# Optimization experiments

Hardware: AMD Instinct MI355X
Metric: run time of the kernel (lower is better)

The kernel has to match this reference:

```python
import jax, jax.numpy as jnp
import numpy as np

NUM_HEADS = 8


def setup_inputs() -> dict:
    key = jax.random.key(0)
    ks = jax.random.split(key, 8)
    B, S, D = 2, 4096, 512
    # Linear weights init uniform(-0.1, 0.1), no bias; stored as [in, out]
    u = lambda k, shp: jax.random.uniform(k, shp, jnp.float32, -0.1, 0.1)
    return {
        "query_antecedent": jax.random.normal(ks[0], (B, S, D), jnp.float32),
        "memory_antecedent": jax.random.normal(ks[1], (B, S, D), jnp.float32),
        "bias": jax.random.normal(ks[2], (1, S, S), jnp.float32),
        "Wq": u(ks[3], (D, D)),
        "Wk": u(ks[4], (D, D)),
        "Wv": u(ks[5], (D, D)),
        "Wo": u(ks[6], (D, D)),
    }


def reference(query_antecedent, memory_antecedent, bias, Wq, Wk, Wv, Wo):
    B, S, D = query_antecedent.shape
    H = NUM_HEADS
    hd = D // H
    scale = hd ** (-0.5)
    q = (query_antecedent @ Wq) * scale              # [B,S,D]
    k = memory_antecedent @ Wk                       # [B,S,D]
    v = memory_antecedent @ Wv                       # [B,S,D]
    q = q.reshape(B, S, H, hd)
    k = k.reshape(B, S, H, hd)
    v = v.reshape(B, S, H, hd)
    # per-head logits with shared bias (broadcast over batch and heads)
    logits = jnp.einsum("bqhd,bkhd->bhqk", q, k) + bias[:, None, :, :]
    weights = jax.nn.softmax(logits, axis=-1)        # [B,H,S,S]
    out = jnp.einsum("bhqk,bkhd->bqhd", weights, v).reshape(B, S, D)
    return out @ Wo
```

## Files before the change

### kernel.cpp

```cpp
#include <hip/hip_runtime.h>
#include <hip/hip_bf16.h>

typedef __attribute__((ext_vector_type(8))) __bf16 bf16x8;
typedef __attribute__((ext_vector_type(4))) __bf16 bf16x4;
typedef __attribute__((ext_vector_type(4))) float f32x4;

#define LOG2E 1.4426950408889634f
#define FIXED_M 16.0f

static __device__ __forceinline__ f32x4 mfma16(bf16x8 a, bf16x8 b, f32x4 c) {
  return __builtin_amdgcn_mfma_f32_16x16x32_bf16(a, b, c, 0, 0, 0);
}

static __device__ __forceinline__ void gload_lds16(const void* g, void* l) {
  __builtin_amdgcn_global_load_lds(
      (const __attribute__((address_space(1))) unsigned int*)g,
      (__attribute__((address_space(3))) unsigned int*)l, 16, 0, 0);
}

__global__ __launch_bounds__(256) void k_cvt(const float* __restrict__ in,
                                             __bf16* __restrict__ out, int n4) {
  for (int i = blockIdx.x * blockDim.x + threadIdx.x; i < n4;
       i += gridDim.x * blockDim.x) {
    float4 v = reinterpret_cast<const float4*>(in)[i];
    bf16x4 o = {(__bf16)v.x, (__bf16)v.y, (__bf16)v.z, (__bf16)v.w};
    reinterpret_cast<bf16x4*>(out)[i] = o;
  }
}

__global__ __launch_bounds__(256) void k_wt(const float* __restrict__ W,
                                            __bf16* __restrict__ Wt) {
  __shared__ float tile[64][65];
  int bx = blockIdx.x;
  int by = blockIdx.y;
  int tid = threadIdx.x;
#pragma unroll
  for (int p = 0; p < 16; p++) {
    int idx = p * 256 + tid;
    int r = idx >> 6, c = idx & 63;
    tile[r][c] = W[(size_t)(by * 64 + r) * 512 + bx * 64 + c];
  }
  __syncthreads();
#pragma unroll
  for (int p = 0; p < 16; p++) {
    int idx = p * 256 + tid;
    int rn = idx >> 6, ck = idx & 63;
    Wt[(size_t)(bx * 64 + rn) * 512 + by * 64 + ck] = (__bf16)tile[ck][rn];
  }
}

template <int OUT_MODE>
__global__ __launch_bounds__(256) void k_gemm(const __bf16* __restrict__ A,
                                              const __bf16* __restrict__ Bt,
                                              void* __restrict__ Cout,
                                              float scale) {
  constexpr bool SWAP = (OUT_MODE != 2);
  __shared__ __bf16 As[128][72];
  __shared__ __bf16 Bs[64][72];
  const int tid = threadIdx.x;
  const int wid = tid >> 6, lane = tid & 63;
  const int g = lane >> 4, c = lane & 15;
  const int m0 = blockIdx.x * 128, n0 = blockIdx.y * 64;
  const int wr = wid >> 1, wc = wid & 1;

  f32x4 acc[4][2];
#pragma unroll
  for (int i = 0; i < 4; i++)
#pragma unroll
    for (int j = 0; j < 2; j++) acc[i][j] = (f32x4){0.f, 0.f, 0.f, 0.f};

  for (int k0 = 0; k0 < 512; k0 += 64) {
#pragma unroll
    for (int q = 0; q < 4; q++) {
      int idx = (q * 256 + tid) * 8;
      int r = idx >> 6, cc = idx & 63;
      bf16x8 v = *reinterpret_cast<const bf16x8*>(A + (size_t)(m0 + r) * 512 + k0 + cc);
      *reinterpret_cast<bf16x8*>(&As[r][cc]) = v;
    }
#pragma unroll
    for (int q = 0; q < 2; q++) {
      int idx = (q * 256 + tid) * 8;
      int r = idx >> 6, cc = idx & 63;
      bf16x8 v = *reinterpret_cast<const bf16x8*>(Bt + (size_t)(n0 + r) * 512 + k0 + cc);
      *reinterpret_cast<bf16x8*>(&Bs[r][cc]) = v;
    }
    __syncthreads();
#pragma unroll
    for (int kk = 0; kk < 2; kk++) {
      bf16x8 bfrag[2];
#pragma unroll
      for (int nf = 0; nf < 2; nf++)
        bfrag[nf] = *reinterpret_cast<const bf16x8*>(&Bs[wc * 32 + nf * 16 + c][kk * 32 + g * 8]);
#pragma unroll
      for (int mf = 0; mf < 4; mf++) {
        bf16x8 afrag = *reinterpret_cast<const bf16x8*>(&As[wr * 64 + mf * 16 + c][kk * 32 + g * 8]);
#pragma unroll
        for (int nf = 0; nf < 2; nf++)
          acc[mf][nf] = SWAP ? mfma16(bfrag[nf], afrag, acc[mf][nf])
                             : mfma16(afrag, bfrag[nf], acc[mf][nf]);
      }
    }
    __syncthreads();
  }
#pragma unroll
  for (int mf = 0; mf < 4; mf++)
#pragma unroll
    for (int nf = 0; nf < 2; nf++) {
      if (OUT_MODE == 0) {
        int mm = m0 + wr * 64 + mf * 16 + c;
        int nnb = n0 + wc * 32 + nf * 16 + g * 4;
        int b = mm >> 12, s = mm & 4095, h = nnb >> 6, d = nnb & 63;
        bf16x4 ov = {(__bf16)(acc[mf][nf][0] * scale), (__bf16)(acc[mf][nf][1] * scale),
                     (__bf16)(acc[mf][nf][2] * scale), (__bf16)(acc[mf][nf][3] * scale)};
        *reinterpret_cast<bf16x4*>((__bf16*)Cout + ((((size_t)b * 8 + h) * 4096) + s) * 64 + d) = ov;
      } else if (OUT_MODE == 1) {
        int mm = m0 + wr * 64 + mf * 16 + c;
        int nnb = n0 + wc * 32 + nf * 16 + g * 4;
        f32x4 ov = acc[mf][nf] * scale;
        *reinterpret_cast<f32x4*>((float*)Cout + (size_t)mm * 512 + nnb) = ov;
      } else {
        int mmb = m0 + wr * 64 + mf * 16 + g * 4;
        int nn = n0 + wc * 32 + nf * 16 + c;
        int b = mmb >> 12, s = mmb & 4095, h = nn >> 6, d = nn & 63;
        bf16x4 ov = {(__bf16)(acc[mf][nf][0] * scale), (__bf16)(acc[mf][nf][1] * scale),
                     (__bf16)(acc[mf][nf][2] * scale), (__bf16)(acc[mf][nf][3] * scale)};
        *reinterpret_cast<bf16x4*>((__bf16*)Cout + (((size_t)b * 8 + h) * 64 + d) * 4096 + s) = ov;
      }
    }
}

__global__ __launch_bounds__(256, 2) void k_attn(const __bf16* __restrict__ Q,
                                                 const __bf16* __restrict__ K,
                                                 const __bf16* __restrict__ Vt,
                                                 const float* __restrict__ bias,
                                                 __bf16* __restrict__ Out) {
  __shared__ __bf16 KVs[2][2][64][64];
  __shared__ __bf16 Pl[4][2][16][64];

  const int qb = blockIdx.x, bh = blockIdx.y;
  const int b = bh >> 3, h = bh & 7;
  const int tid = threadIdx.x, wid = tid >> 6, lane = tid & 63;
  const int g = lane >> 4, c = lane & 15;
  const int swz = (c & 7) << 4;
  const char* Kb = (const char*)(K + (size_t)bh * 4096 * 64);
  const char* Vb = (const char*)(Vt + (size_t)bh * 64 * 4096);
  const __bf16* Qh = Q + (size_t)bh * 4096 * 64;
  const int q0 = qb * 128 + wid * 32;
  const int myq0 = q0 + c, myq1 = q0 + 16 + c;

  auto stage = [&](int db, int chunk) {
    const int reg = wid >> 1;
    char* dst0 = (char*)&KVs[db][reg][0][0] + (wid & 1) * 4096;
#pragma unroll
    for (int j = 0; j < 4; j++) {
      int Lp = (wid & 1) * 4096 + j * 1024 + lane * 16;
      int L = Lp ^ (((Lp >> 7) & 7) << 4);
      const char* src = (reg == 0)
          ? Kb + (size_t)chunk * 8192 + L
          : Vb + (size_t)(L >> 7) * 8192 + (size_t)chunk * 128 + (L & 127);
      gload_lds16(src, dst0 + j * 1024);
    }
  };

  const float* brow0 = bias + (size_t)myq0 * 4096;
  const float* brow1 = bias + (size_t)myq1 * 4096;

#define LOADB(dst, chunk)                                                      \
  {                                                                            \
    _Pragma("unroll") for (int f = 0; f < 4; f++) dst[0][f] =                  \
        *reinterpret_cast<const f32x4*>(brow0 + (chunk) * 64 + f * 16 + g * 4);\
    _Pragma("unroll") for (int f = 0; f < 4; f++) dst[1][f] =                  \
        *reinterpret_cast<const f32x4*>(brow1 + (chunk) * 64 + f * 16 + g * 4);\
  }

  bf16x8 qa[2][2];
  qa[0][0] = *reinterpret_cast<const bf16x8*>(Qh + (size_t)myq0 * 64 + g * 8);
  qa[0][1] = *reinterpret_cast<const bf16x8*>(Qh + (size_t)myq0 * 64 + 32 + g * 8);
  qa[1][0] = *reinterpret_cast<const bf16x8*>(Qh + (size_t)myq1 * 64 + g * 8);
  qa[1][1] = *reinterpret_cast<const bf16x8*>(Qh + (size_t)myq1 * 64 + 32 + g * 8);

  f32x4 lacc[2];
  lacc[0] = (f32x4){0.f, 0.f, 0.f, 0.f};
  lacc[1] = (f32x4){0.f, 0.f, 0.f, 0.f};
  f32x4 o[2][4];
#pragma unroll
  for (int qt = 0; qt < 2; qt++)
#pragma unroll
    for (int f = 0; f < 4; f++) o[qt][f] = (f32x4){0.f, 0.f, 0.f, 0.f};

  f32x4 bA[2][4], bB[2][4];
  const float NM = -FIXED_M * LOG2E;

  auto process = [&](int db, f32x4 (&bv)[2][4]) {
    asm volatile("s_waitcnt vmcnt(12)" ::: "memory");
    __builtin_amdgcn_s_barrier();
    const char* Kl = (const char*)&KVs[db][0][0][0];
    const char* Vl = (const char*)&KVs[db][1][0][0];
    f32x4 st[2][4];
    __builtin_amdgcn_s_setprio(1);
#pragma unroll
    for (int f = 0; f < 4; f++) {
      const char* rb = Kl + (f * 16 + c) * 128;
      bf16x8 k0 = *reinterpret_cast<const bf16x8*>(rb + ((g * 16) ^ swz));
      bf16x8 k1 = *reinterpret_cast<const bf16x8*>(rb + ((64 + g * 16) ^ swz));
      st[0][f] = mfma16(k1, qa[0][1], mfma16(k0, qa[0][0], bv[0][f]));
      st[1][f] = mfma16(k1, qa[1][1], mfma16(k0, qa[1][0], bv[1][f]));
    }
    __builtin_amdgcn_s_setprio(0);
#pragma unroll
    for (int qt = 0; qt < 2; qt++) {
      char* Pw = (char*)&Pl[wid][qt][0][0] + c * 128;
#pragma unroll
      for (int f = 0; f < 4; f++) {
#pragma unroll
        for (int r = 0; r < 4; r++)
          st[qt][f][r] = __builtin_exp2f(__builtin_fmaf(st[qt][f][r], LOG2E, NM));
        lacc[qt] += st[qt][f];
        bf16x4 pk = {(__bf16)st[qt][f][0], (__bf16)st[qt][f][1],
                     (__bf16)st[qt][f][2], (__bf16)st[qt][f][3]};
        *reinterpret_cast<bf16x4*>(Pw + ((f * 32 + g * 8) ^ swz)) = pk;
      }
    }
    __builtin_amdgcn_s_setprio(1);
#pragma unroll
    for (int kk = 0; kk < 2; kk++) {
      bf16x8 pb0 = *reinterpret_cast<const bf16x8*>(
          (char*)&Pl[wid][0][0][0] + c * 128 + ((kk * 64 + g * 16) ^ swz));
      bf16x8 pb1 = *reinterpret_cast<const bf16x8*>(
          (char*)&Pl[wid][1][0][0] + c * 128 + ((kk * 64 + g * 16) ^ swz));
#pragma unroll
      for (int fd = 0; fd < 4; fd++) {
        const char* rb = Vl + (fd * 16 + c) * 128;
        bf16x8 va = *reinterpret_cast<const bf16x8*>(rb + ((kk * 64 + g * 16) ^ swz));
        o[0][fd] = mfma16(va, pb0, o[0][fd]);
        o[1][fd] = mfma16(va, pb1, o[1][fd]);
      }
    }
    __builtin_amdgcn_s_setprio(0);
    __builtin_amdgcn_s_barrier();
  };

  stage(0, 0);
  asm volatile("" ::: "memory");
  stage(1, 1);
  asm volatile("" ::: "memory");
  LOADB(bA, 0);
  asm volatile("" ::: "memory");
  LOADB(bB, 1);
  asm volatile("" ::: "memory");

  for (int t = 0; t < 64; t += 2) {
    process(0, bA);
    stage(0, (t + 2) & 63);
    asm volatile("" ::: "memory");
    LOADB(bA, ((t + 2) & 63));
    asm volatile("" ::: "memory");
    process(1, bB);
    stage(1, (t + 3) & 63);
    asm volatile("" ::: "memory");
    LOADB(bB, ((t + 3) & 63));
    asm volatile("" ::: "memory");
  }

#pragma unroll
  for (int qt = 0; qt < 2; qt++) {
    float l = lacc[qt][0] + lacc[qt][1] + lacc[qt][2] + lacc[qt][3];
    l += __shfl_xor(l, 16);
    l += __shfl_xor(l, 32);
    float inv = 1.f / l;
    int myq = (qt == 0) ? myq0 : myq1;
    __bf16* Orow = Out + ((size_t)b * 4096 + myq) * 512 + h * 64;
#pragma unroll
    for (int fd = 0; fd < 4; fd++) {
      bf16x4 ov = {(__bf16)(o[qt][fd][0] * inv), (__bf16)(o[qt][fd][1] * inv),
                   (__bf16)(o[qt][fd][2] * inv), (__bf16)(o[qt][fd][3] * inv)};
      *reinterpret_cast<bf16x4*>(Orow + fd * 16 + g * 4) = ov;
    }
  }
#undef LOADB
}

extern "C" void kernel_launch(void* const* d_in, const int* in_sizes, int n_in,
                              void* d_out, int out_size, void* d_ws, size_t ws_size,
                              hipStream_t stream) {
  const float* xq = (const float*)d_in[0];
  const float* xm = (const float*)d_in[1];
  const float* bias = (const float*)d_in[2];
  const float* Wq = (const float*)d_in[3];
  const float* Wk = (const float*)d_in[4];
  const float* Wv = (const float*)d_in[5];
  const float* Wo = (const float*)d_in[6];

  const size_t MB = 1024 * 1024;
  char* ws = (char*)d_ws;
  __bf16* xq_b = (__bf16*)(ws + 0);
  __bf16* xm_b = (__bf16*)(ws + 8 * MB);
  __bf16* wqt = (__bf16*)(ws + 16 * MB);
  __bf16* wkt = (__bf16*)(ws + 16 * MB + 524288);
  __bf16* wvt = (__bf16*)(ws + 17 * MB);
  __bf16* wot = (__bf16*)(ws + 17 * MB + 524288);
  __bf16* Qb = (__bf16*)(ws + 18 * MB);
  __bf16* Kb = (__bf16*)(ws + 26 * MB);
  __bf16* Vtb = (__bf16*)(ws + 42 * MB);
  __bf16* AOb = (__bf16*)(ws + 50 * MB);
  if (ws_size < 58 * MB) return;

  const int n4 = 8192 * 512 / 4;
  k_cvt<<<2048, 256, 0, stream>>>(xq, xq_b, n4);
  k_cvt<<<2048, 256, 0, stream>>>(xm, xm_b, n4);
  k_wt<<<dim3(8, 8), 256, 0, stream>>>(Wq, wqt);
  k_wt<<<dim3(8, 8), 256, 0, stream>>>(Wk, wkt);
  k_wt<<<dim3(8, 8), 256, 0, stream>>>(Wv, wvt);
  k_wt<<<dim3(8, 8), 256, 0, stream>>>(Wo, wot);

  k_gemm<0><<<dim3(64, 8), 256, 0, stream>>>(xq_b, wqt, Qb, 0.125f);
  k_gemm<0><<<dim3(64, 8), 256, 0, stream>>>(xm_b, wkt, Kb, 1.0f);
  k_gemm<2><<<dim3(64, 8), 256, 0, stream>>>(xm_b, wvt, Vtb, 1.0f);

  k_attn<<<dim3(32, 16), 256, 0, stream>>>(Qb, Kb, Vtb, bias, AOb);

  k_gemm<1><<<dim3(64, 8), 256, 0, stream>>>(AOb, wot, d_out, 1.0f);
}
```

Before: 233.6 us.

## Split attention over key range into two halves with a reduction kernel

The attention grid gains a z dimension that splits the 4096 keys into two halves. Each block writes unnormalized bf16 partial outputs and row sums, and a new reduction kernel adds the halves and normalizes. The P tile in shared memory shrinks to one query tile per wave and launch bounds rise to 4 blocks per SM to raise occupancy. The workspace is reused to hold the partials. The cost is an extra launch, more global traffic for the partials, and bf16 rounding of the unnormalized partials.

```diff
diff --git a/kernel.cpp b/kernel.cpp
--- a/kernel.cpp
+++ b/kernel.cpp
@@ -129,16 +129,17 @@
     }
 }
 
-__global__ __launch_bounds__(256, 2) void k_attn(const __bf16* __restrict__ Q,
+__global__ __launch_bounds__(256, 4) void k_attn(const __bf16* __restrict__ Q,
                                                  const __bf16* __restrict__ K,
                                                  const __bf16* __restrict__ Vt,
                                                  const float* __restrict__ bias,
-                                                 __bf16* __restrict__ Out) {
+                                                 __bf16* __restrict__ Opart,
+                                                 float* __restrict__ lpart) {
   __shared__ __bf16 KVs[2][2][64][64];
-  __shared__ __bf16 Pl[4][2][16][64];
-
-  const int qb = blockIdx.x, bh = blockIdx.y;
-  const int b = bh >> 3, h = bh & 7;
+  __shared__ __bf16 Pl[4][16][64];
+
+  const int qb = blockIdx.x, bh = blockIdx.y, kh = blockIdx.z;
+  const int kb0 = kh * 32;
   const int tid = threadIdx.x, wid = tid >> 6, lane = tid & 63;
   const int g = lane >> 4, c = lane & 15;
   const int swz = (c & 7) << 4;
@@ -207,9 +208,9 @@
       st[1][f] = mfma16(k1, qa[1][1], mfma16(k0, qa[1][0], bv[1][f]));
     }
     __builtin_amdgcn_s_setprio(0);
+    char* Pw = (char*)&Pl[wid][0][0] + c * 128;
 #pragma unroll
     for (int qt = 0; qt < 2; qt++) {
-      char* Pw = (char*)&Pl[wid][qt][0][0] + c * 128;
 #pragma unroll
       for (int f = 0; f < 4; f++) {
 #pragma unroll
@@ -220,45 +221,41 @@
                      (__bf16)st[qt][f][2], (__bf16)st[qt][f][3]};
         *reinterpret_cast<bf16x4*>(Pw + ((f * 32 + g * 8) ^ swz)) = pk;
       }
-    }
-    __builtin_amdgcn_s_setprio(1);
-#pragma unroll
-    for (int kk = 0; kk < 2; kk++) {
-      bf16x8 pb0 = *reinterpret_cast<const bf16x8*>(
-          (char*)&Pl[wid][0][0][0] + c * 128 + ((kk * 64 + g * 16) ^ swz));
-      bf16x8 pb1 = *reinterpret_cast<const bf16x8*>(
-          (char*)&Pl[wid][1][0][0] + c * 128 + ((kk * 64 + g * 16) ^ swz));
-#pragma unroll
-      for (int fd = 0; fd < 4; fd++) {
-        const char* rb = Vl + (fd * 16 + c) * 128;
-        bf16x8 va = *reinterpret_cast<const bf16x8*>(rb + ((kk * 64 + g * 16) ^ swz));
-        o[0][fd] = mfma16(va, pb0, o[0][fd]);
-        o[1][fd] = mfma16(va, pb1, o[1][fd]);
+      __builtin_amdgcn_s_setprio(1);
+#pragma unroll
+      for (int kk = 0; kk < 2; kk++) {
+        bf16x8 pb = *reinterpret_cast<const bf16x8*>(Pw + ((kk * 64 + g * 16) ^ swz));
+#pragma unroll
+        for (int fd = 0; fd < 4; fd++) {
+          const char* rb = Vl + (fd * 16 + c) * 128;
+          bf16x8 va = *reinterpret_cast<const bf16x8*>(rb + ((kk * 64 + g * 16) ^ swz));
+          o[qt][fd] = mfma16(va, pb, o[qt][fd]);
+        }
       }
-    }
-    __builtin_amdgcn_s_setprio(0);
+      __builtin_amdgcn_s_setprio(0);
+    }
     __builtin_amdgcn_s_barrier();
   };
 
-  stage(0, 0);
+  stage(0, kb0 + 0);
   asm volatile("" ::: "memory");
-  stage(1, 1);
+  stage(1, kb0 + 1);
   asm volatile("" ::: "memory");
-  LOADB(bA, 0);
+  LOADB(bA, kb0 + 0);
   asm volatile("" ::: "memory");
-  LOADB(bB, 1);
+  LOADB(bB, kb0 + 1);
   asm volatile("" ::: "memory");
 
-  for (int t = 0; t < 64; t += 2) {
+  for (int t = 0; t < 32; t += 2) {
     process(0, bA);
-    stage(0, (t + 2) & 63);
+    stage(0, kb0 + ((t + 2) & 31));
     asm volatile("" ::: "memory");
-    LOADB(bA, ((t + 2) & 63));
+    LOADB(bA, kb0 + ((t + 2) & 31));
     asm volatile("" ::: "memory");
     process(1, bB);
-    stage(1, (t + 3) & 63);
+    stage(1, kb0 + ((t + 3) & 31));
     asm volatile("" ::: "memory");
-    LOADB(bB, ((t + 3) & 63));
+    LOADB(bB, kb0 + ((t + 3) & 31));
     asm volatile("" ::: "memory");
   }
 
@@ -267,17 +264,40 @@
     float l = lacc[qt][0] + lacc[qt][1] + lacc[qt][2] + lacc[qt][3];
     l += __shfl_xor(l, 16);
     l += __shfl_xor(l, 32);
-    float inv = 1.f / l;
     int myq = (qt == 0) ? myq0 : myq1;
-    __bf16* Orow = Out + ((size_t)b * 4096 + myq) * 512 + h * 64;
+    __bf16* Oprow = Opart + (((size_t)kh * 16 + bh) * 4096 + myq) * 64;
 #pragma unroll
     for (int fd = 0; fd < 4; fd++) {
-      bf16x4 ov = {(__bf16)(o[qt][fd][0] * inv), (__bf16)(o[qt][fd][1] * inv),
-                   (__bf16)(o[qt][fd][2] * inv), (__bf16)(o[qt][fd][3] * inv)};
-      *reinterpret_cast<bf16x4*>(Orow + fd * 16 + g * 4) = ov;
-    }
+      bf16x4 ov = {(__bf16)o[qt][fd][0], (__bf16)o[qt][fd][1],
+                   (__bf16)o[qt][fd][2], (__bf16)o[qt][fd][3]};
+      *reinterpret_cast<bf16x4*>(Oprow + fd * 16 + g * 4) = ov;
+    }
+    if (g == 0) lpart[((size_t)kh * 16 + bh) * 4096 + myq] = l;
   }
 #undef LOADB
+}
+
+__global__ __launch_bounds__(256) void k_red(const __bf16* __restrict__ Op,
+                                             const float* __restrict__ lp,
+                                             __bf16* __restrict__ AO) {
+  int i = blockIdx.x * 256 + threadIdx.x;
+  int bh = i >> 16;
+  int rem = i & 65535;
+  int s = rem >> 4;
+  int d4 = (rem & 15) << 2;
+  int b = bh >> 3, h = bh & 7;
+  size_t base0 = ((size_t)bh * 4096 + s) * 64 + d4;
+  size_t base1 = ((size_t)(16 + bh) * 4096 + s) * 64 + d4;
+  bf16x4 a = *reinterpret_cast<const bf16x4*>(Op + base0);
+  bf16x4 cc = *reinterpret_cast<const bf16x4*>(Op + base1);
+  float la = lp[(size_t)bh * 4096 + s];
+  float lb = lp[(size_t)(16 + bh) * 4096 + s];
+  float inv = 1.f / (la + lb);
+  bf16x4 ov = {(__bf16)(((float)a[0] + (float)cc[0]) * inv),
+               (__bf16)(((float)a[1] + (float)cc[1]) * inv),
+               (__bf16)(((float)a[2] + (float)cc[2]) * inv),
+               (__bf16)(((float)a[3] + (float)cc[3]) * inv)};
+  *reinterpret_cast<bf16x4*>(AO + ((size_t)b * 4096 + s) * 512 + h * 64 + d4) = ov;
 }
 
 extern "C" void kernel_launch(void* const* d_in, const int* in_sizes, int n_in,
@@ -295,15 +315,17 @@
   char* ws = (char*)d_ws;
   __bf16* xq_b = (__bf16*)(ws + 0);
   __bf16* xm_b = (__bf16*)(ws + 8 * MB);
+  __bf16* Opart = (__bf16*)(ws + 0);
   __bf16* wqt = (__bf16*)(ws + 16 * MB);
+  float* lpart = (float*)(ws + 16 * MB);
   __bf16* wkt = (__bf16*)(ws + 16 * MB + 524288);
   __bf16* wvt = (__bf16*)(ws + 17 * MB);
   __bf16* wot = (__bf16*)(ws + 17 * MB + 524288);
   __bf16* Qb = (__bf16*)(ws + 18 * MB);
   __bf16* Kb = (__bf16*)(ws + 26 * MB);
+  __bf16* AOb = (__bf16*)(ws + 34 * MB);
   __bf16* Vtb = (__bf16*)(ws + 42 * MB);
-  __bf16* AOb = (__bf16*)(ws + 50 * MB);
-  if (ws_size < 58 * MB) return;
+  if (ws_size < 50 * MB) return;
 
   const int n4 = 8192 * 512 / 4;
   k_cvt<<<2048, 256, 0, stream>>>(xq, xq_b, n4);
@@ -317,7 +339,8 @@
   k_gemm<0><<<dim3(64, 8), 256, 0, stream>>>(xm_b, wkt, Kb, 1.0f);
   k_gemm<2><<<dim3(64, 8), 256, 0, stream>>>(xm_b, wvt, Vtb, 1.0f);
 
-  k_attn<<<dim3(32, 16), 256, 0, stream>>>(Qb, Kb, Vtb, bias, AOb);
+  k_attn<<<dim3(32, 16, 2), 256, 0, stream>>>(Qb, Kb, Vtb, bias, Opart, lpart);
+  k_red<<<4096, 256, 0, stream>>>(Opart, lpart, AOb);
 
   k_gemm<1><<<dim3(64, 8), 256, 0, stream>>>(AOb, wot, d_out, 1.0f);
 }
```

New measurement: 537.0 us. +129.8%, slower.

## Replace LDS-staged attention with single-wave blocks loading K/V directly into registers

Applied to the files above, without the earlier changes.

Rewrites the attention kernel to use 64-thread blocks, each handling 32 queries. K, V and bias fragments now go straight from global memory into registers with double buffering, replacing the global-to-LDS staging, barriers and 64-key chunks with 32-key chunks. Block ids are remapped so neighbouring blocks cover different heads. This removes block-wide barriers and LDS traffic for K/V, but blocks no longer share K/V in LDS, so global and L2 load traffic rises. Workspace layout is also shrunk.

```diff
diff --git a/kernel.cpp b/kernel.cpp
--- a/kernel.cpp
+++ b/kernel.cpp
@@ -10,12 +10,6 @@
 
 static __device__ __forceinline__ f32x4 mfma16(bf16x8 a, bf16x8 b, f32x4 c) {
   return __builtin_amdgcn_mfma_f32_16x16x32_bf16(a, b, c, 0, 0, 0);
-}
-
-static __device__ __forceinline__ void gload_lds16(const void* g, void* l) {
-  __builtin_amdgcn_global_load_lds(
-      (const __attribute__((address_space(1))) unsigned int*)g,
-      (__attribute__((address_space(3))) unsigned int*)l, 16, 0, 0);
 }
 
 __global__ __launch_bounds__(256) void k_cvt(const float* __restrict__ in,
@@ -129,49 +123,27 @@
     }
 }
 
-__global__ __launch_bounds__(256, 2) void k_attn(const __bf16* __restrict__ Q,
-                                                 const __bf16* __restrict__ K,
-                                                 const __bf16* __restrict__ Vt,
-                                                 const float* __restrict__ bias,
-                                                 __bf16* __restrict__ Out) {
-  __shared__ __bf16 KVs[2][2][64][64];
-  __shared__ __bf16 Pl[4][2][16][64];
-
-  const int qb = blockIdx.x, bh = blockIdx.y;
+__global__ __launch_bounds__(64) void k_attn(const __bf16* __restrict__ Q,
+                                             const __bf16* __restrict__ K,
+                                             const __bf16* __restrict__ Vt,
+                                             const float* __restrict__ bias,
+                                             __bf16* __restrict__ Out) {
+  __shared__ __bf16 Pl[16][64];
+
+  const int id = blockIdx.x;
+  const int bh = ((id & 7) << 1) | ((id >> 3) & 1);
+  const int qb = id >> 4;
   const int b = bh >> 3, h = bh & 7;
-  const int tid = threadIdx.x, wid = tid >> 6, lane = tid & 63;
+  const int lane = threadIdx.x;
   const int g = lane >> 4, c = lane & 15;
   const int swz = (c & 7) << 4;
-  const char* Kb = (const char*)(K + (size_t)bh * 4096 * 64);
-  const char* Vb = (const char*)(Vt + (size_t)bh * 64 * 4096);
+  const __bf16* Kh = K + (size_t)bh * 4096 * 64;
+  const __bf16* Vh = Vt + (size_t)bh * 64 * 4096;
   const __bf16* Qh = Q + (size_t)bh * 4096 * 64;
-  const int q0 = qb * 128 + wid * 32;
+  const int q0 = qb * 32;
   const int myq0 = q0 + c, myq1 = q0 + 16 + c;
-
-  auto stage = [&](int db, int chunk) {
-    const int reg = wid >> 1;
-    char* dst0 = (char*)&KVs[db][reg][0][0] + (wid & 1) * 4096;
-#pragma unroll
-    for (int j = 0; j < 4; j++) {
-      int Lp = (wid & 1) * 4096 + j * 1024 + lane * 16;
-      int L = Lp ^ (((Lp >> 7) & 7) << 4);
-      const char* src = (reg == 0)
-          ? Kb + (size_t)chunk * 8192 + L
-          : Vb + (size_t)(L >> 7) * 8192 + (size_t)chunk * 128 + (L & 127);
-      gload_lds16(src, dst0 + j * 1024);
-    }
-  };
-
   const float* brow0 = bias + (size_t)myq0 * 4096;
   const float* brow1 = bias + (size_t)myq1 * 4096;
-
-#define LOADB(dst, chunk)                                                      \
-  {                                                                            \
-    _Pragma("unroll") for (int f = 0; f < 4; f++) dst[0][f] =                  \
-        *reinterpret_cast<const f32x4*>(brow0 + (chunk) * 64 + f * 16 + g * 4);\
-    _Pragma("unroll") for (int f = 0; f < 4; f++) dst[1][f] =                  \
-        *reinterpret_cast<const f32x4*>(brow1 + (chunk) * 64 + f * 16 + g * 4);\
-  }
 
   bf16x8 qa[2][2];
   qa[0][0] = *reinterpret_cast<const bf16x8*>(Qh + (size_t)myq0 * 64 + g * 8);
@@ -188,78 +160,80 @@
 #pragma unroll
     for (int f = 0; f < 4; f++) o[qt][f] = (f32x4){0.f, 0.f, 0.f, 0.f};
 
-  f32x4 bA[2][4], bB[2][4];
   const float NM = -FIXED_M * LOG2E;
 
-  auto process = [&](int db, f32x4 (&bv)[2][4]) {
-    asm volatile("s_waitcnt vmcnt(12)" ::: "memory");
-    __builtin_amdgcn_s_barrier();
-    const char* Kl = (const char*)&KVs[db][0][0][0];
-    const char* Vl = (const char*)&KVs[db][1][0][0];
-    f32x4 st[2][4];
+  auto loadKB = [&](bf16x8 (&kf)[2][2], f32x4 (&bq)[2][2], int ck) {
+    const __bf16* kp = Kh + (size_t)ck * 32 * 64;
+#pragma unroll
+    for (int f = 0; f < 2; f++) {
+      kf[f][0] = *reinterpret_cast<const bf16x8*>(kp + (size_t)(f * 16 + c) * 64 + g * 8);
+      kf[f][1] = *reinterpret_cast<const bf16x8*>(kp + (size_t)(f * 16 + c) * 64 + 32 + g * 8);
+    }
+#pragma unroll
+    for (int f = 0; f < 2; f++) {
+      bq[0][f] = *reinterpret_cast<const f32x4*>(brow0 + ck * 32 + f * 16 + g * 4);
+      bq[1][f] = *reinterpret_cast<const f32x4*>(brow1 + ck * 32 + f * 16 + g * 4);
+    }
+  };
+  auto loadV = [&](bf16x8 (&vf)[4], int ck) {
+#pragma unroll
+    for (int fd = 0; fd < 4; fd++)
+      vf[fd] = *reinterpret_cast<const bf16x8*>(Vh + (size_t)(fd * 16 + c) * 4096 + ck * 32 + g * 8);
+  };
+
+  auto proc = [&](bf16x8 (&kf)[2][2], bf16x8 (&vf)[4], f32x4 (&bq)[2][2], int nck) {
+    f32x4 st[2][2];
+    st[0][0] = bq[0][0]; st[0][1] = bq[0][1];
+    st[1][0] = bq[1][0]; st[1][1] = bq[1][1];
     __builtin_amdgcn_s_setprio(1);
 #pragma unroll
-    for (int f = 0; f < 4; f++) {
-      const char* rb = Kl + (f * 16 + c) * 128;
-      bf16x8 k0 = *reinterpret_cast<const bf16x8*>(rb + ((g * 16) ^ swz));
-      bf16x8 k1 = *reinterpret_cast<const bf16x8*>(rb + ((64 + g * 16) ^ swz));
-      st[0][f] = mfma16(k1, qa[0][1], mfma16(k0, qa[0][0], bv[0][f]));
-      st[1][f] = mfma16(k1, qa[1][1], mfma16(k0, qa[1][0], bv[1][f]));
+    for (int f = 0; f < 2; f++) {
+      st[0][f] = mfma16(kf[f][1], qa[0][1], mfma16(kf[f][0], qa[0][0], st[0][f]));
+      st[1][f] = mfma16(kf[f][1], qa[1][1], mfma16(kf[f][0], qa[1][0], st[1][f]));
     }
     __builtin_amdgcn_s_setprio(0);
-#pragma unroll
-    for (int qt = 0; qt < 2; qt++) {
-      char* Pw = (char*)&Pl[wid][qt][0][0] + c * 128;
-#pragma unroll
-      for (int f = 0; f < 4; f++) {
+    asm volatile("" ::: "memory");
+    loadKB(kf, bq, nck);
+    asm volatile("" ::: "memory");
+    char* Pw = (char*)&Pl[0][0] + c * 128;
+#pragma unroll
+    for (int qt = 0; qt < 2; qt++)
+#pragma unroll
+      for (int f = 0; f < 2; f++) {
 #pragma unroll
         for (int r = 0; r < 4; r++)
           st[qt][f][r] = __builtin_exp2f(__builtin_fmaf(st[qt][f][r], LOG2E, NM));
         lacc[qt] += st[qt][f];
         bf16x4 pk = {(__bf16)st[qt][f][0], (__bf16)st[qt][f][1],
                      (__bf16)st[qt][f][2], (__bf16)st[qt][f][3]};
-        *reinterpret_cast<bf16x4*>(Pw + ((f * 32 + g * 8) ^ swz)) = pk;
+        *reinterpret_cast<bf16x4*>(Pw + ((qt * 64 + f * 32 + g * 8) ^ swz)) = pk;
       }
-    }
     __builtin_amdgcn_s_setprio(1);
 #pragma unroll
-    for (int kk = 0; kk < 2; kk++) {
-      bf16x8 pb0 = *reinterpret_cast<const bf16x8*>(
-          (char*)&Pl[wid][0][0][0] + c * 128 + ((kk * 64 + g * 16) ^ swz));
-      bf16x8 pb1 = *reinterpret_cast<const bf16x8*>(
-          (char*)&Pl[wid][1][0][0] + c * 128 + ((kk * 64 + g * 16) ^ swz));
-#pragma unroll
-      for (int fd = 0; fd < 4; fd++) {
-        const char* rb = Vl + (fd * 16 + c) * 128;
-        bf16x8 va = *reinterpret_cast<const bf16x8*>(rb + ((kk * 64 + g * 16) ^ swz));
-        o[0][fd] = mfma16(va, pb0, o[0][fd]);
-        o[1][fd] = mfma16(va, pb1, o[1][fd]);
-      }
+    for (int qt = 0; qt < 2; qt++) {
+      bf16x8 pb = *reinterpret_cast<const bf16x8*>(Pw + ((qt * 64 + g * 16) ^ swz));
+#pragma unroll
+      for (int fd = 0; fd < 4; fd++) o[qt][fd] = mfma16(vf[fd], pb, o[qt][fd]);
     }
     __builtin_amdgcn_s_setprio(0);
-    __builtin_amdgcn_s_barrier();
+    asm volatile("" ::: "memory");
+    loadV(vf, nck);
+    asm volatile("" ::: "memory");
   };
 
-  stage(0, 0);
+  bf16x8 kfA[2][2], kfB[2][2], vfA[4], vfB[4];
+  f32x4 bqA[2][2], bqB[2][2];
+
   asm volatile("" ::: "memory");
-  stage(1, 1);
+  loadKB(kfA, bqA, 0);
+  loadV(vfA, 0);
+  loadKB(kfB, bqB, 1);
+  loadV(vfB, 1);
   asm volatile("" ::: "memory");
-  LOADB(bA, 0);
-  asm volatile("" ::: "memory");
-  LOADB(bB, 1);
-  asm volatile("" ::: "memory");
-
-  for (int t = 0; t < 64; t += 2) {
-    process(0, bA);
-    stage(0, (t + 2) & 63);
-    asm volatile("" ::: "memory");
-    LOADB(bA, ((t + 2) & 63));
-    asm volatile("" ::: "memory");
-    process(1, bB);
-    stage(1, (t + 3) & 63);
-    asm volatile("" ::: "memory");
-    LOADB(bB, ((t + 3) & 63));
-    asm volatile("" ::: "memory");
+
+  for (int t = 0; t < 128; t += 2) {
+    proc(kfA, vfA, bqA, (t + 2) & 127);
+    proc(kfB, vfB, bqB, (t + 3) & 127);
   }
 
 #pragma unroll
@@ -277,7 +251,6 @@
       *reinterpret_cast<bf16x4*>(Orow + fd * 16 + g * 4) = ov;
     }
   }
-#undef LOADB
 }
 
 extern "C" void kernel_launch(void* const* d_in, const int* in_sizes, int n_in,
@@ -301,9 +274,9 @@
   __bf16* wot = (__bf16*)(ws + 17 * MB + 524288);
   __bf16* Qb = (__bf16*)(ws + 18 * MB);
   __bf16* Kb = (__bf16*)(ws + 26 * MB);
+  __bf16* AOb = (__bf16*)(ws + 34 * MB);
   __bf16* Vtb = (__bf16*)(ws + 42 * MB);
-  __bf16* AOb = (__bf16*)(ws + 50 * MB);
-  if (ws_size < 58 * MB) return;
+  if (ws_size < 50 * MB) return;
 
   const int n4 = 8192 * 512 / 4;
   k_cvt<<<2048, 256, 0, stream>>>(xq, xq_b, n4);
@@ -317,7 +290,7 @@
   k_gemm<0><<<dim3(64, 8), 256, 0, stream>>>(xm_b, wkt, Kb, 1.0f);
   k_gemm<2><<<dim3(64, 8), 256, 0, stream>>>(xm_b, wvt, Vtb, 1.0f);
 
-  k_attn<<<dim3(32, 16), 256, 0, stream>>>(Qb, Kb, Vtb, bias, AOb);
+  k_attn<<<2048, 64, 0, stream>>>(Qb, Kb, Vtb, bias, AOb);
 
   k_gemm<1><<<dim3(64, 8), 256, 0, stream>>>(AOb, wot, d_out, 1.0f);
 }
```

Result: slower. 414.2 us (+77.3%).
